# Performance work log

Measured on AMD Instinct MI355X. Metric: run time of the kernel, lower is better.

## Reference

```python
import jax, jax.numpy as jnp
import numpy as np

T, I, H, C = 2048, 1024, 1024, 1000


def _lstm(x, W_ih, W_hh, b_ih, b_hh):
    # x: [T, I]; PyTorch LSTM gate order: i, f, g, o
    x_proj = x @ W_ih.T + b_ih + b_hh  # [T, 4H] input projection hoisted out of scan
    h_dim = W_hh.shape[1]

    def step(carry, xp):
        h, c = carry
        gates = xp + h @ W_hh.T  # [4H]
        i, f, g, o = jnp.split(gates, 4)
        i = jax.nn.sigmoid(i)
        f = jax.nn.sigmoid(f)
        g = jnp.tanh(g)
        o = jax.nn.sigmoid(o)
        c_new = f * c + i * g
        h_new = o * jnp.tanh(c_new)
        return (h_new, c_new), h_new

    h0 = jnp.zeros((h_dim,), x.dtype)
    (_, _), hs = jax.lax.scan(step, (h0, h0), x_proj)
    return hs  # [T, H]


def setup_inputs() -> dict:
    key = jax.random.key(0)
    ks = jax.random.split(key, 12)
    s = 1.0 / np.sqrt(H)  # torch LSTM uniform(-1/sqrt(H), 1/sqrt(H)) scale
    u = lambda k, shape: jax.random.uniform(k, shape, jnp.float32, -s, s)
    return {
        "x": jax.random.normal(ks[0], (T, I), jnp.float32),
        "W_ih_f": u(ks[1], (4 * H, I)),
        "W_hh_f": u(ks[2], (4 * H, H)),
        "b_ih_f": u(ks[3], (4 * H,)),
        "b_hh_f": u(ks[4], (4 * H,)),
        "W_ih_b": u(ks[5], (4 * H, I)),
        "W_hh_b": u(ks[6], (4 * H, H)),
        "b_ih_b": u(ks[7], (4 * H,)),
        "b_hh_b": u(ks[8], (4 * H,)),
        "fc_W": u(ks[9], (C, 2 * H)),
        "fc_b": u(ks[10], (C,)),
    }


def reference(x, W_ih_f, W_hh_f, b_ih_f, b_hh_f, W_ih_b, W_hh_b, b_ih_b, b_hh_b, fc_W, fc_b):
    h_fwd = _lstm(x, W_ih_f, W_hh_f, b_ih_f, b_hh_f)            # [T, H]
    h_bwd = _lstm(x[::-1], W_ih_b, W_hh_b, b_ih_b, b_hh_b)[::-1]  # [T, H], re-reversed
    h = jnp.concatenate([h_fwd, h_bwd], axis=-1)                  # [T, 2H]
    return h @ fc_W.T + fc_b                                      # [T, C]
```

## Files before the change

kernel.cpp:

```cpp
#include <hip/hip_runtime.h>
#include <hip/hip_bf16.h>
#include <cstdint>


typedef __fp16 h2 __attribute__((ext_vector_type(2)));
typedef __fp16 h8 __attribute__((ext_vector_type(8)));
typedef float f4 __attribute__((ext_vector_type(4)));
typedef unsigned long long u64;

#define T_LEN 2048

static __device__ __forceinline__ unsigned int packh2(float a, float b) {
  h2 r = __builtin_amdgcn_cvt_pkrtz(a, b);
  return __builtin_bit_cast(unsigned int, r);
}
static __device__ __forceinline__ float fdot2u(unsigned int a, unsigned int b, float c) {
  return __builtin_amdgcn_fdot2(__builtin_bit_cast(h2, a), __builtin_bit_cast(h2, b), c, false);
}
static __device__ __forceinline__ float sigmoidf_(float x) {
  return 1.f / (1.f + __expf(-x));
}
static __device__ __forceinline__ float tanhf_(float x) {
  float e = __expf(-2.f * fabsf(x));
  float r = (1.f - e) / (1.f + e);
  return copysignf(r, x);
}

__global__ void convert_all(const float* __restrict__ x, const float* __restrict__ wf,
                            const float* __restrict__ wb, const float* __restrict__ fcw,
                            _Float16* __restrict__ xf, _Float16* __restrict__ wff,
                            _Float16* __restrict__ wbf, _Float16* __restrict__ fcwf) {
  const size_t SX = 2097152, SW = 4194304, SFC = 2097152;
  size_t i = (size_t)blockIdx.x * 256 + threadIdx.x;
  if (i < SX) {
    xf[i] = (_Float16)x[i];
  } else if (i < SX + SW) {
    size_t j = i - SX; wff[j] = (_Float16)wf[j];
  } else if (i < SX + 2 * SW) {
    size_t j = i - SX - SW; wbf[j] = (_Float16)wb[j];
  } else if (i < SX + 2 * SW + SFC) {
    size_t j = i - SX - 2 * SW;
    int row = (int)(j >> 11), col = (int)(j & 2047);
    fcwf[j] = (row < 1000) ? (_Float16)fcw[(size_t)row * 2048 + col] : (_Float16)0.f;
  }
}

__global__ void init_state(u64* __restrict__ hc) {
  int t = threadIdx.x;
  for (int i = t; i < 2048; i += 256) hc[i] = 0ull;
}

#define LSTR 80

template <int MODE>
__global__ __launch_bounds__(256, 2) void gemm_f16(
    const _Float16* __restrict__ A, const _Float16* __restrict__ B,
    const float* __restrict__ bias1, const float* __restrict__ bias2,
    void* __restrict__ Cout, int M, int N, int K, int nout, int rev) {
  __shared__ _Float16 As[128 * LSTR];
  __shared__ _Float16 Bs[128 * LSTR];

  const int tid = threadIdx.x;
  const int ntn = N >> 7;
  const int tm = blockIdx.x / ntn, tn = blockIdx.x % ntn;
  const int wid = tid >> 6, lane = tid & 63;
  const int wr = wid >> 1, wc = wid & 1;
  const int quad = lane >> 4, l16 = lane & 15;

  const int srow = tid >> 1, seg = tid & 1;
  const int arow = rev ? (M - 1 - (tm * 128 + srow)) : (tm * 128 + srow);
  const int brow = tn * 128 + srow;

  f4 acc[4][4];
#pragma unroll
  for (int i = 0; i < 4; ++i)
#pragma unroll
    for (int j = 0; j < 4; ++j) acc[i][j] = (f4)0.f;

  for (int k0 = 0; k0 < K; k0 += 64) {
    uint4 va[4], vb[4];
    const uint4* gpa = (const uint4*)(A + (size_t)arow * K + k0 + seg * 32);
    const uint4* gpb = (const uint4*)(B + (size_t)brow * K + k0 + seg * 32);
#pragma unroll
    for (int c = 0; c < 4; ++c) va[c] = gpa[c];
#pragma unroll
    for (int c = 0; c < 4; ++c) vb[c] = gpb[c];

    __syncthreads();
    uint4* lpa = (uint4*)&As[srow * LSTR + seg * 32];
    uint4* lpb = (uint4*)&Bs[srow * LSTR + seg * 32];
#pragma unroll
    for (int c = 0; c < 4; ++c) lpa[c] = va[c];
#pragma unroll
    for (int c = 0; c < 4; ++c) lpb[c] = vb[c];
    __syncthreads();

#pragma unroll
    for (int kk = 0; kk < 64; kk += 32) {
      h8 af[4], bf[4];
#pragma unroll
      for (int i = 0; i < 4; ++i) {
        int m = wr * 64 + i * 16 + l16;
        af[i] = *(const h8*)&As[m * LSTR + kk + quad * 8];
        int n = wc * 64 + i * 16 + l16;
        bf[i] = *(const h8*)&Bs[n * LSTR + kk + quad * 8];
      }
#pragma unroll
      for (int i = 0; i < 4; ++i)
#pragma unroll
        for (int j = 0; j < 4; ++j)
          acc[i][j] = __builtin_amdgcn_mfma_f32_16x16x32_f16(af[i], bf[j], acc[i][j], 0, 0, 0);
    }
  }

  const int cm0 = tm * 128 + wr * 64, cn0 = tn * 128 + wc * 64;
#pragma unroll
  for (int i = 0; i < 4; ++i) {
#pragma unroll
    for (int j = 0; j < 4; ++j) {
      int n = cn0 + j * 16 + l16;
#pragma unroll
      for (int r = 0; r < 4; ++r) {
        int m = cm0 + i * 16 + quad * 4 + r;
        float v = acc[i][j][r];
        if (MODE == 0) {
          v += bias1[n] + bias2[n];
          ((_Float16*)Cout)[(size_t)m * N + n] = (_Float16)v;
        } else {
          if (n < nout) ((float*)Cout)[(size_t)m * nout + n] = v + bias1[n];
        }
      }
    }
  }
}

__global__ __launch_bounds__(256, 1) void lstm_rec(
    const float* __restrict__ Whh_f, const float* __restrict__ Whh_b,
    const _Float16* __restrict__ xp,
    u64* __restrict__ hc,
    _Float16* __restrict__ hhist) {
  const int tid = threadIdx.x;
  const int blk = blockIdx.x;
  const int dir = blk >> 6;
  const int ib = blk & 63;
  const int j0 = ib * 16;
  const int wv = tid >> 6;
  const int l = tid & 63;
  const int g = l >> 4;
  const int kq = l & 15;
  const int q = l & 3;
  const int wrow0 = g * 1024 + j0 + 4 * wv;

  const float* Whh = dir ? Whh_b : Whh_f;
  const _Float16* xpd = xp + (size_t)dir * (2048u * 4096u);

  __shared__ unsigned int lds_h[2][16 * 36];
  __shared__ float lds_tr[4 * 16];

  unsigned int w[4][32];
#pragma unroll
  for (int j = 0; j < 4; ++j) {
    const float* wp = Whh + (size_t)(wrow0 + j) * 1024 + kq * 64;
#pragma unroll
    for (int i = 0; i < 16; ++i) {
      float4 v = ((const float4*)wp)[i];
      w[j][2 * i] = packh2(v.x, v.y);
      w[j][2 * i + 1] = packh2(v.z, v.w);
    }
  }

  float c = 0.f;

  uint2 xv = *(const uint2*)(xpd + wrow0);
  h2 x01 = __builtin_bit_cast(h2, xv.x);
  h2 x23 = __builtin_bit_cast(h2, xv.y);
  float xf[4] = {(float)x01[0], (float)x01[1], (float)x23[0], (float)x23[1]};

  for (int t = 0; t < T_LEN; ++t) {
    const int buf = t & 1;
    unsigned d0, d1;
    {
      u64* src = hc + (((size_t)buf * 2 + dir) * 512 + 2 * tid);
      u64 a = __hip_atomic_load(&src[0], __ATOMIC_RELAXED, __HIP_MEMORY_SCOPE_AGENT);
      u64 b = __hip_atomic_load(&src[1], __ATOMIC_RELAXED, __HIP_MEMORY_SCOPE_AGENT);
      int cnt = 0;
      while ((unsigned)a != (unsigned)t || (unsigned)b != (unsigned)t) {
        if (++cnt > (1 << 12)) break;
        a = __hip_atomic_load(&src[0], __ATOMIC_RELAXED, __HIP_MEMORY_SCOPE_AGENT);
        b = __hip_atomic_load(&src[1], __ATOMIC_RELAXED, __HIP_MEMORY_SCOPE_AGENT);
      }
      d0 = (unsigned)(a >> 32);
      d1 = (unsigned)(b >> 32);
    }

    int tnx = (t + 1 < T_LEN) ? t + 1 : t;
    uint2 xn = *(const uint2*)(xpd + (size_t)tnx * 4096 + wrow0);

    *(uint2*)&lds_h[buf][(tid >> 4) * 36 + 2 * (tid & 15)] = make_uint2(d0, d1);
    __syncthreads();

    float acc0 = 0.f, acc1 = 0.f, acc2 = 0.f, acc3 = 0.f;
    const uint4* hp = (const uint4*)&lds_h[buf][kq * 36];
#pragma unroll
    for (int i = 0; i < 8; ++i) {
      uint4 hv = hp[i];
      acc0 = fdot2u(w[0][4 * i + 0], hv.x, acc0);
      acc0 = fdot2u(w[0][4 * i + 1], hv.y, acc0);
      acc0 = fdot2u(w[0][4 * i + 2], hv.z, acc0);
      acc0 = fdot2u(w[0][4 * i + 3], hv.w, acc0);
      acc1 = fdot2u(w[1][4 * i + 0], hv.x, acc1);
      acc1 = fdot2u(w[1][4 * i + 1], hv.y, acc1);
      acc1 = fdot2u(w[1][4 * i + 2], hv.z, acc1);
      acc1 = fdot2u(w[1][4 * i + 3], hv.w, acc1);
      acc2 = fdot2u(w[2][4 * i + 0], hv.x, acc2);
      acc2 = fdot2u(w[2][4 * i + 1], hv.y, acc2);
      acc2 = fdot2u(w[2][4 * i + 2], hv.z, acc2);
      acc2 = fdot2u(w[2][4 * i + 3], hv.w, acc2);
      acc3 = fdot2u(w[3][4 * i + 0], hv.x, acc3);
      acc3 = fdot2u(w[3][4 * i + 1], hv.y, acc3);
      acc3 = fdot2u(w[3][4 * i + 2], hv.z, acc3);
      acc3 = fdot2u(w[3][4 * i + 3], hv.w, acc3);
    }
#pragma unroll
    for (int m = 1; m < 16; m <<= 1) {
      acc0 += __shfl_xor(acc0, m, 64);
      acc1 += __shfl_xor(acc1, m, 64);
      acc2 += __shfl_xor(acc2, m, 64);
      acc3 += __shfl_xor(acc3, m, 64);
    }

    if (kq == 0) {
      f4 v = {acc0 + xf[0], acc1 + xf[1], acc2 + xf[2], acc3 + xf[3]};
      *(f4*)&lds_tr[wv * 16 + g * 4] = v;
    }
    float pi = lds_tr[wv * 16 + 0 + q];
    float pf = lds_tr[wv * 16 + 4 + q];
    float pg = lds_tr[wv * 16 + 8 + q];
    float po = lds_tr[wv * 16 + 12 + q];

    float ii = sigmoidf_(pi);
    float ff = sigmoidf_(pf);
    float g_ = tanhf_(pg);
    float oo = sigmoidf_(po);
    c = ff * c + ii * g_;
    float h = oo * tanhf_(c);

    float h1 = __shfl(h, 1, 64);
    float h2v = __shfl(h, 2, 64);
    float h3 = __shfl(h, 3, 64);
    if (l == 0) {
      unsigned p01 = packh2(h, h1);
      unsigned p23 = packh2(h2v, h3);
      u64 w0 = ((u64)p01 << 32) | (unsigned)(t + 1);
      u64 w1 = ((u64)p23 << 32) | (unsigned)(t + 1);
      u64* dst = hc + (((size_t)((t + 1) & 1) * 2 + dir) * 512 + (ib * 8 + 2 * wv));
      __hip_atomic_store(&dst[0], w0, __ATOMIC_RELAXED, __HIP_MEMORY_SCOPE_AGENT);
      __hip_atomic_store(&dst[1], w1, __ATOMIC_RELAXED, __HIP_MEMORY_SCOPE_AGENT);
      int tout = dir ? (T_LEN - 1 - t) : t;
      *(uint2*)&hhist[(size_t)tout * 2048 + dir * 1024 + j0 + 4 * wv] =
          make_uint2(p01, p23);
    }

    x01 = __builtin_bit_cast(h2, xn.x);
    x23 = __builtin_bit_cast(h2, xn.y);
    xf[0] = (float)x01[0]; xf[1] = (float)x01[1];
    xf[2] = (float)x23[0]; xf[3] = (float)x23[1];
  }
}

extern "C" void kernel_launch(void* const* d_in, const int* in_sizes, int n_in,
                              void* d_out, int out_size, void* d_ws, size_t ws_size,
                              hipStream_t stream) {
  (void)in_sizes; (void)n_in; (void)out_size; (void)ws_size;
  const float* x     = (const float*)d_in[0];
  const float* Wih_f = (const float*)d_in[1];
  const float* Whh_f = (const float*)d_in[2];
  const float* bih_f = (const float*)d_in[3];
  const float* bhh_f = (const float*)d_in[4];
  const float* Wih_b = (const float*)d_in[5];
  const float* Whh_b = (const float*)d_in[6];
  const float* bih_b = (const float*)d_in[7];
  const float* bhh_b = (const float*)d_in[8];
  const float* fcW   = (const float*)d_in[9];
  const float* fcb   = (const float*)d_in[10];

  char* ws = (char*)d_ws;
  _Float16* xf16   = (_Float16*)(ws + 0);
  _Float16* wih16f = (_Float16*)(ws + 4194304);
  _Float16* wih16b = (_Float16*)(ws + 12582912);
  _Float16* fcw16  = (_Float16*)(ws + 20971520);
  _Float16* xp16   = (_Float16*)(ws + 25165824);
  _Float16* hhist  = (_Float16*)(ws + 58720256);
  u64*      hc     = (u64*)     (ws + 67108864);

  const size_t SX = 2097152, SW = 4194304, SFC = 2097152;
  const size_t total_cvt = SX + 2 * SW + SFC;

  convert_all<<<dim3((unsigned)((total_cvt + 255) / 256)), 256, 0, stream>>>(
      x, Wih_f, Wih_b, fcW, xf16, wih16f, wih16b, fcw16);
  init_state<<<1, 256, 0, stream>>>(hc);

  gemm_f16<0><<<dim3(512), 256, 0, stream>>>(xf16, wih16f, bih_f, bhh_f,
                                             (void*)xp16, 2048, 4096, 1024, 4096, 0);
  gemm_f16<0><<<dim3(512), 256, 0, stream>>>(xf16, wih16b, bih_b, bhh_b,
                                             (void*)(xp16 + (size_t)2048 * 4096),
                                             2048, 4096, 1024, 4096, 1);

  lstm_rec<<<dim3(128), 256, 0, stream>>>(Whh_f, Whh_b, xp16, hc, hhist);

  gemm_f16<1><<<dim3(128), 256, 0, stream>>>(hhist, fcw16, fcb, nullptr,
                                             d_out, 2048, 1024, 2048, 1000, 0);
}
```

Before: 3.736 ms.

## Vectorize conversion, merge input-projection GEMMs, pipeline spin-wait polling loads

The fp32-to-fp16 conversion kernel now handles four elements per thread with float4 loads and packed half stores. The forward and backward input-projection GEMMs become one launch of 1024 blocks, with direction chosen by the block index parity. The recurrent kernel's spin-wait keeps four pairs of agent-scope loads in flight, so a fresh hidden state should be seen sooner each step. The per-step latency of the 2048-step recurrence dominates, so gains come mainly from the polling change, which adds memory traffic on the flag lines.

Measured after the change: 4.281 ms. 1.15x slower.

```diff
diff --git a/kernel.cpp b/kernel.cpp
--- a/kernel.cpp
+++ b/kernel.cpp
@@ -24,6 +24,9 @@
   float e = __expf(-2.f * fabsf(x));
   float r = (1.f - e) / (1.f + e);
   return copysignf(r, x);
+}
+static __device__ __forceinline__ u64 ld_agent(const u64* p) {
+  return __hip_atomic_load(p, __ATOMIC_RELAXED, __HIP_MEMORY_SCOPE_AGENT);
 }
 
 __global__ void convert_all(const float* __restrict__ x, const float* __restrict__ wf,
@@ -31,17 +34,24 @@
                             _Float16* __restrict__ xf, _Float16* __restrict__ wff,
                             _Float16* __restrict__ wbf, _Float16* __restrict__ fcwf) {
   const size_t SX = 2097152, SW = 4194304, SFC = 2097152;
-  size_t i = (size_t)blockIdx.x * 256 + threadIdx.x;
+  size_t i = ((size_t)blockIdx.x * 256 + threadIdx.x) * 4;
   if (i < SX) {
-    xf[i] = (_Float16)x[i];
+    float4 v = *(const float4*)(x + i);
+    *(uint2*)(xf + i) = make_uint2(packh2(v.x, v.y), packh2(v.z, v.w));
   } else if (i < SX + SW) {
-    size_t j = i - SX; wff[j] = (_Float16)wf[j];
+    size_t j = i - SX;
+    float4 v = *(const float4*)(wf + j);
+    *(uint2*)(wff + j) = make_uint2(packh2(v.x, v.y), packh2(v.z, v.w));
   } else if (i < SX + 2 * SW) {
-    size_t j = i - SX - SW; wbf[j] = (_Float16)wb[j];
+    size_t j = i - SX - SW;
+    float4 v = *(const float4*)(wb + j);
+    *(uint2*)(wbf + j) = make_uint2(packh2(v.x, v.y), packh2(v.z, v.w));
   } else if (i < SX + 2 * SW + SFC) {
     size_t j = i - SX - 2 * SW;
     int row = (int)(j >> 11), col = (int)(j & 2047);
-    fcwf[j] = (row < 1000) ? (_Float16)fcw[(size_t)row * 2048 + col] : (_Float16)0.f;
+    float4 v = make_float4(0.f, 0.f, 0.f, 0.f);
+    if (row < 1000) v = *(const float4*)(fcw + (size_t)row * 2048 + col);
+    *(uint2*)(fcwf + j) = make_uint2(packh2(v.x, v.y), packh2(v.z, v.w));
   }
 }
 
@@ -54,15 +64,36 @@
 
 template <int MODE>
 __global__ __launch_bounds__(256, 2) void gemm_f16(
-    const _Float16* __restrict__ A, const _Float16* __restrict__ B,
-    const float* __restrict__ bias1, const float* __restrict__ bias2,
-    void* __restrict__ Cout, int M, int N, int K, int nout, int rev) {
+    const _Float16* __restrict__ A, const _Float16* __restrict__ Bf,
+    const _Float16* __restrict__ Bb,
+    const float* __restrict__ b1f, const float* __restrict__ b2f,
+    const float* __restrict__ b1b, const float* __restrict__ b2b,
+    void* __restrict__ Cout, int M, int N, int K, int nout) {
   __shared__ _Float16 As[128 * LSTR];
   __shared__ _Float16 Bs[128 * LSTR];
 
+  int bid, dirv;
+  const _Float16* B;
+  const float* bias1;
+  const float* bias2;
+  if (MODE == 0) {
+    dirv = blockIdx.x & 1;
+    bid = blockIdx.x >> 1;
+    B = dirv ? Bb : Bf;
+    bias1 = dirv ? b1b : b1f;
+    bias2 = dirv ? b2b : b2f;
+  } else {
+    dirv = 0;
+    bid = blockIdx.x;
+    B = Bf;
+    bias1 = b1f;
+    bias2 = nullptr;
+  }
+  const int rev = (MODE == 0) ? dirv : 0;
+
   const int tid = threadIdx.x;
   const int ntn = N >> 7;
-  const int tm = blockIdx.x / ntn, tn = blockIdx.x % ntn;
+  const int tm = bid / ntn, tn = bid % ntn;
   const int wid = tid >> 6, lane = tid & 63;
   const int wr = wid >> 1, wc = wid & 1;
   const int quad = lane >> 4, l16 = lane & 15;
@@ -125,7 +156,7 @@
         float v = acc[i][j][r];
         if (MODE == 0) {
           v += bias1[n] + bias2[n];
-          ((_Float16*)Cout)[(size_t)m * N + n] = (_Float16)v;
+          ((_Float16*)Cout)[(size_t)dirv * M * N + (size_t)m * N + n] = (_Float16)v;
         } else {
           if (n < nout) ((float*)Cout)[(size_t)m * nout + n] = v + bias1[n];
         }
@@ -180,17 +211,24 @@
     const int buf = t & 1;
     unsigned d0, d1;
     {
-      u64* src = hc + (((size_t)buf * 2 + dir) * 512 + 2 * tid);
-      u64 a = __hip_atomic_load(&src[0], __ATOMIC_RELAXED, __HIP_MEMORY_SCOPE_AGENT);
-      u64 b = __hip_atomic_load(&src[1], __ATOMIC_RELAXED, __HIP_MEMORY_SCOPE_AGENT);
+      const u64* src = hc + (((size_t)buf * 2 + dir) * 512 + 2 * tid);
+      const unsigned tt = (unsigned)t;
+      u64 a0 = ld_agent(&src[0]), b0 = ld_agent(&src[1]);
+      u64 a1 = ld_agent(&src[0]), b1 = ld_agent(&src[1]);
+      u64 a2 = ld_agent(&src[0]), b2 = ld_agent(&src[1]);
+      u64 a3 = ld_agent(&src[0]), b3 = ld_agent(&src[1]);
       int cnt = 0;
-      while ((unsigned)a != (unsigned)t || (unsigned)b != (unsigned)t) {
-        if (++cnt > (1 << 12)) break;
-        a = __hip_atomic_load(&src[0], __ATOMIC_RELAXED, __HIP_MEMORY_SCOPE_AGENT);
-        b = __hip_atomic_load(&src[1], __ATOMIC_RELAXED, __HIP_MEMORY_SCOPE_AGENT);
+      while (true) {
+        if ((unsigned)a0 == tt && (unsigned)b0 == tt) { d0 = (unsigned)(a0 >> 32); d1 = (unsigned)(b0 >> 32); break; }
+        a0 = ld_agent(&src[0]); b0 = ld_agent(&src[1]);
+        if ((unsigned)a1 == tt && (unsigned)b1 == tt) { d0 = (unsigned)(a1 >> 32); d1 = (unsigned)(b1 >> 32); break; }
+        a1 = ld_agent(&src[0]); b1 = ld_agent(&src[1]);
+        if ((unsigned)a2 == tt && (unsigned)b2 == tt) { d0 = (unsigned)(a2 >> 32); d1 = (unsigned)(b2 >> 32); break; }
+        a2 = ld_agent(&src[0]); b2 = ld_agent(&src[1]);
+        if ((unsigned)a3 == tt && (unsigned)b3 == tt) { d0 = (unsigned)(a3 >> 32); d1 = (unsigned)(b3 >> 32); break; }
+        a3 = ld_agent(&src[0]); b3 = ld_agent(&src[1]);
+        if (++cnt > (1 << 11)) { d0 = (unsigned)(a0 >> 32); d1 = (unsigned)(b0 >> 32); break; }
       }
-      d0 = (unsigned)(a >> 32);
-      d1 = (unsigned)(b >> 32);
     }
 
     int tnx = (t + 1 < T_LEN) ? t + 1 : t;
@@ -296,18 +334,17 @@
   const size_t SX = 2097152, SW = 4194304, SFC = 2097152;
   const size_t total_cvt = SX + 2 * SW + SFC;
 
-  convert_all<<<dim3((unsigned)((total_cvt + 255) / 256)), 256, 0, stream>>>(
+  convert_all<<<dim3((unsigned)(total_cvt / 4 / 256)), 256, 0, stream>>>(
       x, Wih_f, Wih_b, fcW, xf16, wih16f, wih16b, fcw16);
   init_state<<<1, 256, 0, stream>>>(hc);
 
-  gemm_f16<0><<<dim3(512), 256, 0, stream>>>(xf16, wih16f, bih_f, bhh_f,
-                                             (void*)xp16, 2048, 4096, 1024, 4096, 0);
-  gemm_f16<0><<<dim3(512), 256, 0, stream>>>(xf16, wih16b, bih_b, bhh_b,
-                                             (void*)(xp16 + (size_t)2048 * 4096),
-                                             2048, 4096, 1024, 4096, 1);
+  gemm_f16<0><<<dim3(1024), 256, 0, stream>>>(
+      xf16, wih16f, wih16b, bih_f, bhh_f, bih_b, bhh_b,
+      (void*)xp16, 2048, 4096, 1024, 4096);
 
   lstm_rec<<<dim3(128), 256, 0, stream>>>(Whh_f, Whh_b, xp16, hc, hhist);
 
-  gemm_f16<1><<<dim3(128), 256, 0, stream>>>(hhist, fcw16, fcb, nullptr,
-                                             d_out, 2048, 1024, 2048, 1000, 0);
-}
+  gemm_f16<1><<<dim3(128), 256, 0, stream>>>(
+      hhist, fcw16, nullptr, fcb, nullptr, nullptr, nullptr,
+      d_out, 2048, 1024, 2048, 1000);
+}
```
